# Kernel tuning notes

Hardware: AMD Instinct MI355X
Metric: run time of the kernel (lower is better)

Reference implementation:

```python
import jax, jax.numpy as jnp
import numpy as np

N_NODES = 50000
N_EDGES = 800000
NODE_DIM = 128
EDGE_DIM = 64
HIDDEN = 256


def setup_inputs() -> dict:
    key = jax.random.key(0)
    ks = jax.random.split(key, 12)
    glorot = lambda k, fi, fo: jax.random.normal(k, (fi, fo), jnp.float32) * (2.0 / (fi + fo)) ** 0.5
    return {
        "node_features": jax.random.normal(ks[0], (N_NODES, NODE_DIM), jnp.float32),
        "edge_features": jax.random.normal(ks[1], (N_EDGES, EDGE_DIM), jnp.float32),
        "src": jax.random.randint(ks[2], (N_EDGES,), 0, N_NODES),
        "dst": jax.random.randint(ks[3], (N_EDGES,), 0, N_NODES),
        # edge_update MLP: (2*node_dim + edge_dim) -> hidden -> edge_dim
        "We1": glorot(ks[4], 2 * NODE_DIM + EDGE_DIM, HIDDEN),
        "be1": jnp.zeros((HIDDEN,), jnp.float32),
        "We2": glorot(ks[5], HIDDEN, EDGE_DIM),
        "be2": jnp.zeros((EDGE_DIM,), jnp.float32),
        # node_update MLP: (node_dim + edge_dim) -> hidden -> node_dim
        "Wn1": glorot(ks[6], NODE_DIM + EDGE_DIM, HIDDEN),
        "bn1": jnp.zeros((HIDDEN,), jnp.float32),
        "Wn2": glorot(ks[7], HIDDEN, NODE_DIM),
        "bn2": jnp.zeros((NODE_DIM,), jnp.float32),
    }


def reference(node_features, edge_features, src, dst, We1, be1, We2, be2, Wn1, bn1, Wn2, bn2):
    # message: per-edge MLP on [src_h, e, dst_h]
    concat = jnp.concatenate(
        [node_features[src], edge_features, node_features[dst]], axis=1
    )  # [E, 2*node_dim + edge_dim]
    e_upd = jax.nn.relu(concat @ We1 + be1) @ We2 + be2  # [E, edge_dim]

    # reduce: sum incoming messages per destination node
    e_sum = jax.ops.segment_sum(e_upd, dst, num_segments=node_features.shape[0])  # [N, edge_dim]
    node_in = jnp.concatenate([node_features, e_sum], axis=1)  # [N, node_dim + edge_dim]
    h_new = jax.nn.relu(node_in @ Wn1 + bn1) @ Wn2 + bn2  # [N, node_dim]

    # DGL only applies reduce_func to nodes with at least one incoming edge
    deg = jax.ops.segment_sum(jnp.ones_like(dst, jnp.float32), dst, num_segments=node_features.shape[0])
    h_out = jnp.where(deg[:, None] > 0, h_new, node_features)

    # original module never writes e_updated back: returned edge features are the inputs
    return h_out, edge_features
```

## Files before the change

kernel.cpp:

```cpp
#include <hip/hip_runtime.h>

#define N_NODES 50000
#define N_EDGES 800000
#define NODE_DIM 128
#define EDGE_DIM 64
#define HIDDEN 256
#define K_E 320
#define K_N 192

typedef __attribute__((ext_vector_type(8))) short bf16x8;
typedef __attribute__((ext_vector_type(4))) float f32x4;
typedef unsigned short u16;
typedef unsigned int u32;

__device__ inline u16 f2bf(float f) {
  u32 u = __builtin_bit_cast(u32, f);
  u += 0x7fffu + ((u >> 16) & 1u);
  return (u16)(u >> 16);
}

__device__ inline void st_bf4(u16* p, float4 v) {
  ushort4 r;
  r.x = f2bf(v.x); r.y = f2bf(v.y); r.z = f2bf(v.z); r.w = f2bf(v.w);
  *reinterpret_cast<ushort4*>(p) = r;
}

__global__ void prep_weights(const float* __restrict__ We1, const float* __restrict__ We2,
                             const float* __restrict__ Wn1, const float* __restrict__ Wn2,
                             u16* __restrict__ we1t, u16* __restrict__ we2t,
                             u16* __restrict__ wn1t, u16* __restrict__ wn2t) {
  const int stride = gridDim.x * blockDim.x;
  const int tid = blockIdx.x * blockDim.x + threadIdx.x;
  for (int i = tid; i < HIDDEN * K_E; i += stride) {
    int n = i / K_E, k = i % K_E;
    we1t[i] = f2bf(We1[k * HIDDEN + n]);
  }
  for (int i = tid; i < EDGE_DIM * HIDDEN; i += stride) {
    int n = i / HIDDEN, k = i % HIDDEN;
    we2t[i] = f2bf(We2[k * EDGE_DIM + n]);
  }
  for (int i = tid; i < HIDDEN * K_N; i += stride) {
    int n = i / K_N, k = i % K_N;
    wn1t[i] = f2bf(Wn1[k * HIDDEN + n]);
  }
  for (int i = tid; i < NODE_DIM * HIDDEN; i += stride) {
    int n = i / HIDDEN, k = i % HIDDEN;
    wn2t[i] = f2bf(Wn2[k * NODE_DIM + n]);
  }
}

#define SA_E 328
#define SH   264

__global__ __launch_bounds__(256) void edge_kernel(
    const float* __restrict__ nf, const float* __restrict__ ef,
    const int* __restrict__ src, const int* __restrict__ dst,
    const u16* __restrict__ w1, const float* __restrict__ b1,
    const u16* __restrict__ w2, const float* __restrict__ b2,
    float* __restrict__ e_sum, float* __restrict__ degf,
    float* __restrict__ out_edge)
{
  __shared__ u16 A[64 * SA_E];
  __shared__ int sidx[64], didx[64];
  const int tid = threadIdx.x;
  const int e0 = blockIdx.x * 64;

  if (tid < 64) { sidx[tid] = src[e0 + tid]; didx[tid] = dst[e0 + tid]; }
  __syncthreads();

  const float4* nf4 = reinterpret_cast<const float4*>(nf);
  const float4* ef4 = reinterpret_cast<const float4*>(ef);
  float4* oe4 = reinterpret_cast<float4*>(out_edge);

  {
    int row = tid >> 5, c4 = tid & 31;
    #pragma unroll
    for (int p = 0; p < 8; ++p, row += 8) {
      float4 v = nf4[(size_t)sidx[row] * 32 + c4];
      st_bf4(&A[row * SA_E + c4 * 4], v);
    }
  }
  {
    #pragma unroll
    for (int p = 0; p < 4; ++p) {
      int idx = p * 256 + tid;
      int row = idx >> 4, c4 = idx & 15;
      size_t g = (size_t)(e0 + row) * 16 + c4;
      float4 v = ef4[g];
      oe4[g] = v;
      st_bf4(&A[row * SA_E + 128 + c4 * 4], v);
    }
  }
  {
    int row = tid >> 5, c4 = tid & 31;
    #pragma unroll
    for (int p = 0; p < 8; ++p, row += 8) {
      float4 v = nf4[(size_t)didx[row] * 32 + c4];
      st_bf4(&A[row * SA_E + 192 + c4 * 4], v);
    }
  }
  if (tid < 64) degf[didx[tid]] = 1.0f;
  __syncthreads();

  const int wave = tid >> 6, lane = tid & 63;
  const int lr = lane & 15;
  const int lk = (lane >> 4) * 8;

  f32x4 acc[4][4] = {};
  for (int kb = 0; kb < K_E / 32; ++kb) {
    const int ko = kb * 32 + lk;
    bf16x8 a[4], b[4];
    #pragma unroll
    for (int mt = 0; mt < 4; ++mt)
      a[mt] = *reinterpret_cast<const bf16x8*>(&A[(mt * 16 + lr) * SA_E + ko]);
    #pragma unroll
    for (int nt = 0; nt < 4; ++nt)
      b[nt] = *reinterpret_cast<const bf16x8*>(&w1[(size_t)(wave * 64 + nt * 16 + lr) * K_E + ko]);
    #pragma unroll
    for (int mt = 0; mt < 4; ++mt)
      #pragma unroll
      for (int nt = 0; nt < 4; ++nt)
        acc[mt][nt] = __builtin_amdgcn_mfma_f32_16x16x32_bf16(a[mt], b[nt], acc[mt][nt], 0, 0, 0);
  }
  __syncthreads();

  u16* H = A;
  #pragma unroll
  for (int mt = 0; mt < 4; ++mt)
    #pragma unroll
    for (int nt = 0; nt < 4; ++nt) {
      int col = wave * 64 + nt * 16 + lr;
      float bias = b1[col];
      #pragma unroll
      for (int j = 0; j < 4; ++j) {
        int row = mt * 16 + (lane >> 4) * 4 + j;
        float h = acc[mt][nt][j] + bias;
        H[row * SH + col] = f2bf(h > 0.f ? h : 0.f);
      }
    }
  __syncthreads();

  f32x4 acc2[4] = {};
  for (int kb = 0; kb < HIDDEN / 32; ++kb) {
    const int ko = kb * 32 + lk;
    bf16x8 a = *reinterpret_cast<const bf16x8*>(&H[(wave * 16 + lr) * SH + ko]);
    #pragma unroll
    for (int nt = 0; nt < 4; ++nt) {
      bf16x8 b = *reinterpret_cast<const bf16x8*>(&w2[(size_t)(nt * 16 + lr) * HIDDEN + ko]);
      acc2[nt] = __builtin_amdgcn_mfma_f32_16x16x32_bf16(a, b, acc2[nt], 0, 0, 0);
    }
  }
  #pragma unroll
  for (int nt = 0; nt < 4; ++nt) {
    int col = nt * 16 + lr;
    float bias = b2[col];
    #pragma unroll
    for (int j = 0; j < 4; ++j) {
      int row = wave * 16 + (lane >> 4) * 4 + j;
      atomicAdd(&e_sum[(size_t)didx[row] * 64 + col], acc2[nt][j] + bias);
    }
  }
}

#define SA_N 200

__global__ __launch_bounds__(256) void node_kernel(
    const float* __restrict__ nf, const float* __restrict__ e_sum,
    const float* __restrict__ degf,
    const u16* __restrict__ w1, const float* __restrict__ b1,
    const u16* __restrict__ w2, const float* __restrict__ b2,
    float* __restrict__ hout)
{
  __shared__ u16 A[64 * SH];
  const int tid = threadIdx.x;
  const int n0 = blockIdx.x * 64;

  const float4* nf4 = reinterpret_cast<const float4*>(nf);
  const float4* es4 = reinterpret_cast<const float4*>(e_sum);

  {
    int row = tid >> 5, c4 = tid & 31;
    #pragma unroll
    for (int p = 0; p < 8; ++p, row += 8) {
      int rg = min(n0 + row, N_NODES - 1);
      float4 v = nf4[(size_t)rg * 32 + c4];
      st_bf4(&A[row * SA_N + c4 * 4], v);
    }
  }
  {
    #pragma unroll
    for (int p = 0; p < 4; ++p) {
      int idx = p * 256 + tid;
      int row = idx >> 4, c4 = idx & 15;
      int rg = min(n0 + row, N_NODES - 1);
      float4 v = es4[(size_t)rg * 16 + c4];
      st_bf4(&A[row * SA_N + 128 + c4 * 4], v);
    }
  }
  __syncthreads();

  const int wave = tid >> 6, lane = tid & 63;
  const int lr = lane & 15;
  const int lk = (lane >> 4) * 8;

  f32x4 acc[4][4] = {};
  for (int kb = 0; kb < K_N / 32; ++kb) {
    const int ko = kb * 32 + lk;
    bf16x8 a[4], b[4];
    #pragma unroll
    for (int mt = 0; mt < 4; ++mt)
      a[mt] = *reinterpret_cast<const bf16x8*>(&A[(mt * 16 + lr) * SA_N + ko]);
    #pragma unroll
    for (int nt = 0; nt < 4; ++nt)
      b[nt] = *reinterpret_cast<const bf16x8*>(&w1[(size_t)(wave * 64 + nt * 16 + lr) * K_N + ko]);
    #pragma unroll
    for (int mt = 0; mt < 4; ++mt)
      #pragma unroll
      for (int nt = 0; nt < 4; ++nt)
        acc[mt][nt] = __builtin_amdgcn_mfma_f32_16x16x32_bf16(a[mt], b[nt], acc[mt][nt], 0, 0, 0);
  }
  __syncthreads();

  u16* H = A;
  #pragma unroll
  for (int mt = 0; mt < 4; ++mt)
    #pragma unroll
    for (int nt = 0; nt < 4; ++nt) {
      int col = wave * 64 + nt * 16 + lr;
      float bias = b1[col];
      #pragma unroll
      for (int j = 0; j < 4; ++j) {
        int row = mt * 16 + (lane >> 4) * 4 + j;
        float h = acc[mt][nt][j] + bias;
        H[row * SH + col] = f2bf(h > 0.f ? h : 0.f);
      }
    }
  __syncthreads();

  f32x4 acc2[8] = {};
  for (int kb = 0; kb < HIDDEN / 32; ++kb) {
    const int ko = kb * 32 + lk;
    bf16x8 a = *reinterpret_cast<const bf16x8*>(&H[(wave * 16 + lr) * SH + ko]);
    #pragma unroll
    for (int nt = 0; nt < 8; ++nt) {
      bf16x8 b = *reinterpret_cast<const bf16x8*>(&w2[(size_t)(nt * 16 + lr) * HIDDEN + ko]);
      acc2[nt] = __builtin_amdgcn_mfma_f32_16x16x32_bf16(a, b, acc2[nt], 0, 0, 0);
    }
  }
  #pragma unroll
  for (int nt = 0; nt < 8; ++nt) {
    int col = nt * 16 + lr;
    float bias = b2[col];
    #pragma unroll
    for (int j = 0; j < 4; ++j) {
      int row = wave * 16 + (lane >> 4) * 4 + j;
      int rg = n0 + row;
      if (rg < N_NODES) {
        float v = acc2[nt][j] + bias;
        hout[(size_t)rg * NODE_DIM + col] =
            (degf[rg] > 0.f) ? v : nf[(size_t)rg * NODE_DIM + col];
      }
    }
  }
}

extern "C" void kernel_launch(void* const* d_in, const int* in_sizes, int n_in,
                              void* d_out, int out_size, void* d_ws, size_t ws_size,
                              hipStream_t stream) {
  const float* nf  = (const float*)d_in[0];
  const float* ef  = (const float*)d_in[1];
  const int*   src = (const int*)d_in[2];
  const int*   dst = (const int*)d_in[3];
  const float* We1 = (const float*)d_in[4];
  const float* be1 = (const float*)d_in[5];
  const float* We2 = (const float*)d_in[6];
  const float* be2 = (const float*)d_in[7];
  const float* Wn1 = (const float*)d_in[8];
  const float* bn1 = (const float*)d_in[9];
  const float* Wn2 = (const float*)d_in[10];
  const float* bn2 = (const float*)d_in[11];

  char* ws = (char*)d_ws;
  float* e_sum = (float*)ws;
  float* degf  = (float*)(ws + 12800000);
  u16*  we1t   = (u16*)(ws + 13000000);
  u16*  we2t   = (u16*)(ws + 13163840);
  u16*  wn1t   = (u16*)(ws + 13196608);
  u16*  wn2t   = (u16*)(ws + 13294912);

  float* hout = (float*)d_out;
  float* out_edge = hout + (size_t)N_NODES * NODE_DIM;

  hipMemsetAsync(ws, 0, 13000000, stream);
  prep_weights<<<128, 256, 0, stream>>>(We1, We2, Wn1, Wn2, we1t, we2t, wn1t, wn2t);
  edge_kernel<<<N_EDGES / 64, 256, 0, stream>>>(nf, ef, src, dst, we1t, be1, we2t, be2,
                                                e_sum, degf, out_edge);
  node_kernel<<<(N_NODES + 63) / 64, 256, 0, stream>>>(nf, e_sum, degf, wn1t, bn1,
                                                       wn2t, bn2, hout);
}
```

Before: 631.3 us.

## Rewrite edge MLP with register-resident inputs and CSR-based segment sum

Replaces the edge kernel with a 32x32 MFMA design. Each lane keeps its edge's gathered input row in registers, and pre-swizzled bf16 W1 tiles are double-buffered through LDS, fusing both MLP layers without staging hidden activations. Node features are pre-converted to bf16 so the gathers move half the bytes. Per-edge outputs are written as bf16 and reduced by a CSR build (histogram, single-block scan, scatter) plus a gather-sum kernel, removing float atomics on e_sum. This adds several extra launches, a serial one-block scan, and a bf16 rounding of the messages before summation.

After: 744.6 us. 1.18x slower.

```diff
diff --git a/kernel.cpp b/kernel.cpp
--- a/kernel.cpp
+++ b/kernel.cpp
@@ -10,15 +10,25 @@
 
 typedef __attribute__((ext_vector_type(8))) short bf16x8;
 typedef __attribute__((ext_vector_type(4))) float f32x4;
+typedef __attribute__((ext_vector_type(16))) float f32x16;
 typedef unsigned short u16;
 typedef unsigned int u32;
+
+#define MFMA16 __builtin_amdgcn_mfma_f32_16x16x32_bf16
+#define MFMA32 __builtin_amdgcn_mfma_f32_32x32x16_bf16
 
 __device__ inline u16 f2bf(float f) {
   u32 u = __builtin_bit_cast(u32, f);
   u += 0x7fffu + ((u >> 16) & 1u);
   return (u16)(u >> 16);
 }
-
+__device__ inline float bf2f(u16 u) {
+  u32 x = ((u32)u) << 16;
+  return __builtin_bit_cast(float, x);
+}
+__device__ inline u32 pack2(float a, float b) {
+  return (u32)f2bf(a) | ((u32)f2bf(b) << 16);
+}
 __device__ inline void st_bf4(u16* p, float4 v) {
   ushort4 r;
   r.x = f2bf(v.x); r.y = f2bf(v.y); r.z = f2bf(v.z); r.w = f2bf(v.w);
@@ -27,17 +37,31 @@
 
 __global__ void prep_weights(const float* __restrict__ We1, const float* __restrict__ We2,
                              const float* __restrict__ Wn1, const float* __restrict__ Wn2,
-                             u16* __restrict__ we1t, u16* __restrict__ we2t,
-                             u16* __restrict__ wn1t, u16* __restrict__ wn2t) {
+                             const float* __restrict__ nf,
+                             u16* __restrict__ w1y, u16* __restrict__ w2y,
+                             u16* __restrict__ wn1t, u16* __restrict__ wn2t,
+                             u16* __restrict__ nfb) {
   const int stride = gridDim.x * blockDim.x;
   const int tid = blockIdx.x * blockDim.x + threadIdx.x;
   for (int i = tid; i < HIDDEN * K_E; i += stride) {
-    int n = i / K_E, k = i % K_E;
-    we1t[i] = f2bf(We1[k * HIDDEN + n]);
+    int jj = i & 7;
+    int l = (i >> 3) & 63;
+    int rem = i % 10240;
+    int kb = rem >> 9;
+    int ht = i / 10240;
+    int h = ht * 32 + (l & 31);
+    int k = kb * 16 + (l >> 5) * 8 + jj;
+    w1y[i] = f2bf(We1[k * HIDDEN + h]);
   }
   for (int i = tid; i < EDGE_DIM * HIDDEN; i += stride) {
-    int n = i / HIDDEN, k = i % HIDDEN;
-    we2t[i] = f2bf(We2[k * EDGE_DIM + n]);
+    int jj = i & 7;
+    int l = (i >> 3) & 63;
+    int t2 = (i >> 9) & 1;
+    int kb2 = i >> 10;
+    int out = t2 * 32 + (l & 31);
+    int hi = l >> 5;
+    int k = kb2 * 16 + (jj & 3) + 8 * (jj >> 2) + 4 * hi;
+    w2y[i] = f2bf(We2[k * EDGE_DIM + out]);
   }
   for (int i = tid; i < HIDDEN * K_N; i += stride) {
     int n = i / K_N, k = i % K_N;
@@ -47,126 +71,208 @@
     int n = i / HIDDEN, k = i % HIDDEN;
     wn2t[i] = f2bf(Wn2[k * NODE_DIM + n]);
   }
-}
-
-#define SA_E 328
+  {
+    const float4* nf4 = reinterpret_cast<const float4*>(nf);
+    for (int i = tid; i < N_NODES * NODE_DIM / 4; i += stride)
+      st_bf4(&nfb[i * 4], nf4[i]);
+  }
+}
+
+__global__ void hist_kernel(const int* __restrict__ dst, int* __restrict__ hist) {
+  int e = blockIdx.x * blockDim.x + threadIdx.x;
+  if (e < N_EDGES) atomicAdd(&hist[dst[e]], 1);
+}
+
+#define SCAN_T 256
+#define SCAN_ITEMS 196
+__global__ void scan_kernel(const int* __restrict__ hist, int* __restrict__ off,
+                            int* __restrict__ cursor) {
+  __shared__ int ssum[SCAN_T];
+  const int tid = threadIdx.x;
+  const int base = tid * SCAN_ITEMS;
+  int s = 0;
+  for (int i = 0; i < SCAN_ITEMS; ++i) {
+    int idx = base + i;
+    s += (idx < N_NODES) ? hist[idx] : 0;
+  }
+  ssum[tid] = s;
+  __syncthreads();
+  for (int d = 1; d < SCAN_T; d <<= 1) {
+    int t = (tid >= d) ? ssum[tid - d] : 0;
+    __syncthreads();
+    ssum[tid] += t;
+    __syncthreads();
+  }
+  int run = ssum[tid] - s;
+  for (int i = 0; i < SCAN_ITEMS; ++i) {
+    int idx = base + i;
+    if (idx < N_NODES) {
+      off[idx] = run;
+      cursor[idx] = run;
+      run += hist[idx];
+    }
+  }
+  if (tid == SCAN_T - 1) off[N_NODES] = run;
+}
+
+__global__ void scatter_kernel(const int* __restrict__ dst, int* __restrict__ cursor,
+                               int* __restrict__ eid) {
+  int e = blockIdx.x * blockDim.x + threadIdx.x;
+  if (e < N_EDGES) eid[atomicAdd(&cursor[dst[e]], 1)] = e;
+}
+
+__global__ __launch_bounds__(256, 3) void edge_mlp(
+    const u16* __restrict__ nfb, const float* __restrict__ ef,
+    const int* __restrict__ src, const int* __restrict__ dst,
+    const u16* __restrict__ w1y, const float* __restrict__ b1,
+    const u16* __restrict__ w2y, const float* __restrict__ b2,
+    u16* __restrict__ e_upd, float* __restrict__ out_edge)
+{
+  __shared__ u16 W1s[2][10240];
+
+  const int tid = threadIdx.x;
+  const int wv = tid >> 6, lane = tid & 63;
+  const int ecol = lane & 31;
+  const int hi = lane >> 5;
+  const int e0 = blockIdx.x * 128;
+  const int eg = e0 + wv * 32 + ecol;
+
+  {
+    const float4* ef4 = reinterpret_cast<const float4*>(ef);
+    float4* oe4 = reinterpret_cast<float4*>(out_edge);
+    #pragma unroll
+    for (int p = 0; p < 8; ++p) {
+      size_t i = (size_t)e0 * 16 + p * 256 + tid;
+      oe4[i] = ef4[i];
+    }
+  }
+
+  const int si = src[eg] << 7;
+  const int di = dst[eg] << 7;
+  bf16x8 efr[20];
+  #pragma unroll
+  for (int kb = 0; kb < 8; ++kb)
+    efr[kb] = *reinterpret_cast<const bf16x8*>(nfb + si + kb * 16 + hi * 8);
+  #pragma unroll
+  for (int kb = 0; kb < 4; ++kb) {
+    const float* ep = ef + (size_t)eg * 64 + kb * 16 + hi * 8;
+    float4 lo = *reinterpret_cast<const float4*>(ep);
+    float4 hv = *reinterpret_cast<const float4*>(ep + 4);
+    bf16x8 v;
+    v[0] = (short)f2bf(lo.x); v[1] = (short)f2bf(lo.y);
+    v[2] = (short)f2bf(lo.z); v[3] = (short)f2bf(lo.w);
+    v[4] = (short)f2bf(hv.x); v[5] = (short)f2bf(hv.y);
+    v[6] = (short)f2bf(hv.z); v[7] = (short)f2bf(hv.w);
+    efr[8 + kb] = v;
+  }
+  #pragma unroll
+  for (int kb = 0; kb < 8; ++kb)
+    efr[12 + kb] = *reinterpret_cast<const bf16x8*>(nfb + di + kb * 16 + hi * 8);
+
+  {
+    const uint4* s = reinterpret_cast<const uint4*>(w1y);
+    uint4* d = reinterpret_cast<uint4*>(W1s[0]);
+    #pragma unroll
+    for (int j = 0; j < 5; ++j) d[tid + j * 256] = s[tid + j * 256];
+  }
+  __syncthreads();
+
+  f32x16 acc2[2];
+  #pragma unroll
+  for (int t2 = 0; t2 < 2; ++t2)
+    #pragma unroll
+    for (int r = 0; r < 16; ++r)
+      acc2[t2][r] = b2[t2 * 32 + (r & 3) + 8 * (r >> 2) + 4 * hi];
+
+  #pragma unroll
+  for (int ht = 0; ht < 8; ++ht) {
+    uint4 st[5];
+    if (ht < 7) {
+      const uint4* s = reinterpret_cast<const uint4*>(w1y + (ht + 1) * 10240);
+      #pragma unroll
+      for (int j = 0; j < 5; ++j) st[j] = s[tid + j * 256];
+    }
+
+    f32x16 acc;
+    #pragma unroll
+    for (int r = 0; r < 16; ++r)
+      acc[r] = b1[ht * 32 + (r & 3) + 8 * (r >> 2) + 4 * hi];
+    const u16* Wb = W1s[ht & 1];
+    #pragma unroll
+    for (int kb = 0; kb < 20; ++kb) {
+      bf16x8 wf = *reinterpret_cast<const bf16x8*>(Wb + (kb * 64 + lane) * 8);
+      acc = MFMA32(wf, efr[kb], acc, 0, 0, 0);
+    }
+
+    #pragma unroll
+    for (int s2 = 0; s2 < 2; ++s2) {
+      bf16x8 hf;
+      u32* hw = reinterpret_cast<u32*>(&hf);
+      #pragma unroll
+      for (int m = 0; m < 4; ++m)
+        hw[m] = pack2(fmaxf(acc[s2 * 8 + 2 * m], 0.f),
+                      fmaxf(acc[s2 * 8 + 2 * m + 1], 0.f));
+      #pragma unroll
+      for (int t2 = 0; t2 < 2; ++t2) {
+        bf16x8 wf2 = *reinterpret_cast<const bf16x8*>(
+            w2y + ((size_t)((ht * 2 + s2) * 2 + t2) * 64 + lane) * 8);
+        acc2[t2] = MFMA32(wf2, hf, acc2[t2], 0, 0, 0);
+      }
+    }
+
+    if (ht < 7) {
+      uint4* d = reinterpret_cast<uint4*>(W1s[(ht + 1) & 1]);
+      #pragma unroll
+      for (int j = 0; j < 5; ++j) d[tid + j * 256] = st[j];
+      __syncthreads();
+    }
+  }
+
+  u16* hb = reinterpret_cast<u16*>(W1s) + wv * 2304;
+  #pragma unroll
+  for (int t2 = 0; t2 < 2; ++t2)
+    #pragma unroll
+    for (int m = 0; m < 8; ++m) {
+      int rowb = 2 * (m & 1) + 8 * (m >> 1) + 4 * hi;
+      *reinterpret_cast<u32*>(hb + ecol * 72 + t2 * 32 + rowb) =
+          pack2(acc2[t2][2 * m], acc2[t2][2 * m + 1]);
+    }
+  {
+    int er = lane >> 1, half = lane & 1;
+    const u16* rp = hb + er * 72 + half * 32;
+    uint4 o0 = *reinterpret_cast<const uint4*>(rp + 0);
+    uint4 o1 = *reinterpret_cast<const uint4*>(rp + 8);
+    uint4 o2 = *reinterpret_cast<const uint4*>(rp + 16);
+    uint4 o3 = *reinterpret_cast<const uint4*>(rp + 24);
+    uint4* dp = reinterpret_cast<uint4*>(
+        e_upd + (size_t)(e0 + wv * 32 + er) * 64 + half * 32);
+    dp[0] = o0; dp[1] = o1; dp[2] = o2; dp[3] = o3;
+  }
+}
+
+__global__ __launch_bounds__(256) void sum_kernel(
+    const u16* __restrict__ e_upd, const int* __restrict__ off,
+    const int* __restrict__ eid, float* __restrict__ e_sum)
+{
+  const int grp = threadIdx.x >> 4, l16 = threadIdx.x & 15;
+  const int n = blockIdx.x * 16 + grp;
+  float4 a = {0.f, 0.f, 0.f, 0.f};
+  const int s0 = off[n], s1 = off[n + 1];
+  for (int s = s0; s < s1; ++s) {
+    int e = eid[s];
+    ushort4 v = *reinterpret_cast<const ushort4*>(&e_upd[(size_t)e * 64 + l16 * 4]);
+    a.x += bf2f(v.x); a.y += bf2f(v.y);
+    a.z += bf2f(v.z); a.w += bf2f(v.w);
+  }
+  *reinterpret_cast<float4*>(&e_sum[(size_t)n * 64 + l16 * 4]) = a;
+}
+
+#define SA_N 200
 #define SH   264
-
-__global__ __launch_bounds__(256) void edge_kernel(
-    const float* __restrict__ nf, const float* __restrict__ ef,
-    const int* __restrict__ src, const int* __restrict__ dst,
-    const u16* __restrict__ w1, const float* __restrict__ b1,
-    const u16* __restrict__ w2, const float* __restrict__ b2,
-    float* __restrict__ e_sum, float* __restrict__ degf,
-    float* __restrict__ out_edge)
-{
-  __shared__ u16 A[64 * SA_E];
-  __shared__ int sidx[64], didx[64];
-  const int tid = threadIdx.x;
-  const int e0 = blockIdx.x * 64;
-
-  if (tid < 64) { sidx[tid] = src[e0 + tid]; didx[tid] = dst[e0 + tid]; }
-  __syncthreads();
-
-  const float4* nf4 = reinterpret_cast<const float4*>(nf);
-  const float4* ef4 = reinterpret_cast<const float4*>(ef);
-  float4* oe4 = reinterpret_cast<float4*>(out_edge);
-
-  {
-    int row = tid >> 5, c4 = tid & 31;
-    #pragma unroll
-    for (int p = 0; p < 8; ++p, row += 8) {
-      float4 v = nf4[(size_t)sidx[row] * 32 + c4];
-      st_bf4(&A[row * SA_E + c4 * 4], v);
-    }
-  }
-  {
-    #pragma unroll
-    for (int p = 0; p < 4; ++p) {
-      int idx = p * 256 + tid;
-      int row = idx >> 4, c4 = idx & 15;
-      size_t g = (size_t)(e0 + row) * 16 + c4;
-      float4 v = ef4[g];
-      oe4[g] = v;
-      st_bf4(&A[row * SA_E + 128 + c4 * 4], v);
-    }
-  }
-  {
-    int row = tid >> 5, c4 = tid & 31;
-    #pragma unroll
-    for (int p = 0; p < 8; ++p, row += 8) {
-      float4 v = nf4[(size_t)didx[row] * 32 + c4];
-      st_bf4(&A[row * SA_E + 192 + c4 * 4], v);
-    }
-  }
-  if (tid < 64) degf[didx[tid]] = 1.0f;
-  __syncthreads();
-
-  const int wave = tid >> 6, lane = tid & 63;
-  const int lr = lane & 15;
-  const int lk = (lane >> 4) * 8;
-
-  f32x4 acc[4][4] = {};
-  for (int kb = 0; kb < K_E / 32; ++kb) {
-    const int ko = kb * 32 + lk;
-    bf16x8 a[4], b[4];
-    #pragma unroll
-    for (int mt = 0; mt < 4; ++mt)
-      a[mt] = *reinterpret_cast<const bf16x8*>(&A[(mt * 16 + lr) * SA_E + ko]);
-    #pragma unroll
-    for (int nt = 0; nt < 4; ++nt)
-      b[nt] = *reinterpret_cast<const bf16x8*>(&w1[(size_t)(wave * 64 + nt * 16 + lr) * K_E + ko]);
-    #pragma unroll
-    for (int mt = 0; mt < 4; ++mt)
-      #pragma unroll
-      for (int nt = 0; nt < 4; ++nt)
-        acc[mt][nt] = __builtin_amdgcn_mfma_f32_16x16x32_bf16(a[mt], b[nt], acc[mt][nt], 0, 0, 0);
-  }
-  __syncthreads();
-
-  u16* H = A;
-  #pragma unroll
-  for (int mt = 0; mt < 4; ++mt)
-    #pragma unroll
-    for (int nt = 0; nt < 4; ++nt) {
-      int col = wave * 64 + nt * 16 + lr;
-      float bias = b1[col];
-      #pragma unroll
-      for (int j = 0; j < 4; ++j) {
-        int row = mt * 16 + (lane >> 4) * 4 + j;
-        float h = acc[mt][nt][j] + bias;
-        H[row * SH + col] = f2bf(h > 0.f ? h : 0.f);
-      }
-    }
-  __syncthreads();
-
-  f32x4 acc2[4] = {};
-  for (int kb = 0; kb < HIDDEN / 32; ++kb) {
-    const int ko = kb * 32 + lk;
-    bf16x8 a = *reinterpret_cast<const bf16x8*>(&H[(wave * 16 + lr) * SH + ko]);
-    #pragma unroll
-    for (int nt = 0; nt < 4; ++nt) {
-      bf16x8 b = *reinterpret_cast<const bf16x8*>(&w2[(size_t)(nt * 16 + lr) * HIDDEN + ko]);
-      acc2[nt] = __builtin_amdgcn_mfma_f32_16x16x32_bf16(a, b, acc2[nt], 0, 0, 0);
-    }
-  }
-  #pragma unroll
-  for (int nt = 0; nt < 4; ++nt) {
-    int col = nt * 16 + lr;
-    float bias = b2[col];
-    #pragma unroll
-    for (int j = 0; j < 4; ++j) {
-      int row = wave * 16 + (lane >> 4) * 4 + j;
-      atomicAdd(&e_sum[(size_t)didx[row] * 64 + col], acc2[nt][j] + bias);
-    }
-  }
-}
-
-#define SA_N 200
 
 __global__ __launch_bounds__(256) void node_kernel(
     const float* __restrict__ nf, const float* __restrict__ e_sum,
-    const float* __restrict__ degf,
+    const int* __restrict__ hist,
     const u16* __restrict__ w1, const float* __restrict__ b1,
     const u16* __restrict__ w2, const float* __restrict__ b2,
     float* __restrict__ hout)
@@ -178,24 +284,21 @@
   const float4* nf4 = reinterpret_cast<const float4*>(nf);
   const float4* es4 = reinterpret_cast<const float4*>(e_sum);
 
-  {
-    int row = tid >> 5, c4 = tid & 31;
-    #pragma unroll
-    for (int p = 0; p < 8; ++p, row += 8) {
-      int rg = min(n0 + row, N_NODES - 1);
-      float4 v = nf4[(size_t)rg * 32 + c4];
-      st_bf4(&A[row * SA_N + c4 * 4], v);
-    }
-  }
-  {
-    #pragma unroll
-    for (int p = 0; p < 4; ++p) {
-      int idx = p * 256 + tid;
-      int row = idx >> 4, c4 = idx & 15;
-      int rg = min(n0 + row, N_NODES - 1);
-      float4 v = es4[(size_t)rg * 16 + c4];
-      st_bf4(&A[row * SA_N + 128 + c4 * 4], v);
-    }
+  #pragma unroll
+  for (int p = 0; p < 8; ++p) {
+    int i = p * 256 + tid;
+    int row = i >> 5, c4 = i & 31;
+    int rg = min(n0 + row, N_NODES - 1);
+    float4 v = nf4[(size_t)rg * 32 + c4];
+    st_bf4(&A[row * SA_N + c4 * 4], v);
+  }
+  #pragma unroll
+  for (int p = 0; p < 4; ++p) {
+    int i = p * 256 + tid;
+    int row = i >> 4, c4 = i & 15;
+    int rg = min(n0 + row, N_NODES - 1);
+    float4 v = es4[(size_t)rg * 16 + c4];
+    st_bf4(&A[row * SA_N + 128 + c4 * 4], v);
   }
   __syncthreads();
 
@@ -217,7 +320,7 @@
     for (int mt = 0; mt < 4; ++mt)
       #pragma unroll
       for (int nt = 0; nt < 4; ++nt)
-        acc[mt][nt] = __builtin_amdgcn_mfma_f32_16x16x32_bf16(a[mt], b[nt], acc[mt][nt], 0, 0, 0);
+        acc[mt][nt] = MFMA16(a[mt], b[nt], acc[mt][nt], 0, 0, 0);
   }
   __syncthreads();
 
@@ -244,7 +347,7 @@
     #pragma unroll
     for (int nt = 0; nt < 8; ++nt) {
       bf16x8 b = *reinterpret_cast<const bf16x8*>(&w2[(size_t)(nt * 16 + lr) * HIDDEN + ko]);
-      acc2[nt] = __builtin_amdgcn_mfma_f32_16x16x32_bf16(a, b, acc2[nt], 0, 0, 0);
+      acc2[nt] = MFMA16(a, b, acc2[nt], 0, 0, 0);
     }
   }
   #pragma unroll
@@ -258,7 +361,7 @@
       if (rg < N_NODES) {
         float v = acc2[nt][j] + bias;
         hout[(size_t)rg * NODE_DIM + col] =
-            (degf[rg] > 0.f) ? v : nf[(size_t)rg * NODE_DIM + col];
+            (hist[rg] != 0) ? v : nf[(size_t)rg * NODE_DIM + col];
       }
     }
   }
@@ -280,21 +383,32 @@
   const float* Wn2 = (const float*)d_in[10];
   const float* bn2 = (const float*)d_in[11];
 
-  char* ws = (char*)d_ws;
-  float* e_sum = (float*)ws;
-  float* degf  = (float*)(ws + 12800000);
-  u16*  we1t   = (u16*)(ws + 13000000);
-  u16*  we2t   = (u16*)(ws + 13163840);
-  u16*  wn1t   = (u16*)(ws + 13196608);
-  u16*  wn2t   = (u16*)(ws + 13294912);
-
   float* hout = (float*)d_out;
   float* out_edge = hout + (size_t)N_NODES * NODE_DIM;
 
-  hipMemsetAsync(ws, 0, 13000000, stream);
-  prep_weights<<<128, 256, 0, stream>>>(We1, We2, Wn1, Wn2, we1t, we2t, wn1t, wn2t);
-  edge_kernel<<<N_EDGES / 64, 256, 0, stream>>>(nf, ef, src, dst, we1t, be1, we2t, be2,
-                                                e_sum, degf, out_edge);
-  node_kernel<<<(N_NODES + 63) / 64, 256, 0, stream>>>(nf, e_sum, degf, wn1t, bn1,
-                                                       wn2t, bn2, hout);
-}
+  char* ws = (char*)d_ws;
+  int* hist    = (int*)ws;
+  int* off     = (int*)(ws + 200000);
+  int* cursor  = (int*)(ws + 400016);
+  int* eid     = (int*)(ws + 600016);
+  u16* e_upd   = (u16*)(ws + 3800016);
+  u16* w1y     = (u16*)(ws + 106200016);
+  u16* w2y     = (u16*)(ws + 106363856);
+  u16* wn1t    = (u16*)(ws + 106396624);
+  u16* wn2t    = (u16*)(ws + 106494928);
+  u16* nfb     = (u16*)(ws + 106560464);
+  float* e_sum = (float*)(ws + 106560464);
+
+  hipMemsetAsync(hist, 0, 200000, stream);
+  prep_weights<<<512, 256, 0, stream>>>(We1, We2, Wn1, Wn2, nf,
+                                        w1y, w2y, wn1t, wn2t, nfb);
+  hist_kernel<<<(N_EDGES + 255) / 256, 256, 0, stream>>>(dst, hist);
+  scan_kernel<<<1, SCAN_T, 0, stream>>>(hist, off, cursor);
+  scatter_kernel<<<(N_EDGES + 255) / 256, 256, 0, stream>>>(dst, cursor, eid);
+
+  edge_mlp<<<N_EDGES / 128, 256, 0, stream>>>(nfb, ef, src, dst, w1y, be1,
+                                              w2y, be2, e_upd, out_edge);
+  sum_kernel<<<N_NODES / 16, 256, 0, stream>>>(e_upd, off, eid, e_sum);
+  node_kernel<<<(N_NODES + 63) / 64, 256, 0, stream>>>(nf, e_sum, hist,
+                                                       wn1t, bn1, wn2t, bn2, hout);
+}
```
